# Kernel optimization log

Measured on AMD Instinct MI355X. Metric: run time of the kernel, lower is better.

## Reference

```python
import jax, jax.numpy as jnp
import numpy as np

B, N, D_IN, D_OUT = 16, 2048, 256, 256

def setup_inputs() -> dict:
    key = jax.random.key(0)
    k1, k2, k3 = jax.random.split(key, 3)
    nodes_rep = jax.random.normal(k1, (B, N, D_IN), dtype=jnp.float32)
    adj_metric = jax.random.uniform(k2, (B, N, N), dtype=jnp.float32)
    # xavier_uniform for [D_IN, D_OUT]
    limit = float(np.sqrt(6.0 / (D_IN + D_OUT)))
    attn_weight = jax.random.uniform(k3, (D_IN, D_OUT), dtype=jnp.float32, minval=-limit, maxval=limit)
    attn_bias = jnp.zeros((D_OUT,), dtype=jnp.float32)
    return {"nodes_rep": nodes_rep, "adj_metric": adj_metric,
            "attn_weight": attn_weight, "attn_bias": attn_bias}

def reference(nodes_rep, adj_metric, attn_weight, attn_bias):
    # h: [B, N, D_OUT]
    h = jnp.einsum('bni,io->bno', nodes_rep, attn_weight)
    # scores: [B, N, N]
    scores = jnp.einsum('bno,bmo->bnm', h, h)
    scores = jax.nn.leaky_relu(scores, negative_slope=0.2)
    scores = scores * adj_metric
    attn = jax.nn.softmax(scores, axis=-1)
    # output aggregates the UNtransformed input, then adds bias
    out = jnp.einsum('bnm,bmd->bnd', attn, nodes_rep) + attn_bias
    return out
```

## Files before the change

### kernel.cpp

```cpp
#include <hip/hip_runtime.h>
#include <math.h>
#include <stdint.h>

typedef _Float16 half8 __attribute__((ext_vector_type(8)));
typedef _Float16 half2v __attribute__((ext_vector_type(2)));
typedef float    f32x4 __attribute__((ext_vector_type(4)));
typedef unsigned int uint4v __attribute__((ext_vector_type(4)));

constexpr int Bc = 16, Nn = 2048, Dd = 256;
constexpr int QTI = 64;
constexpr int MC  = 64;

__device__ _Float16 g_Wt[Dd * Dd];

__global__ void __launch_bounds__(256)
wt_transpose_kernel(const float* __restrict__ W) {
    __shared__ float ts[64][65];
    const int t = threadIdx.x;
    const int r0 = blockIdx.x * 64;
    const int c0 = blockIdx.y * 64;
    for (int idx = t; idx < 64 * 64; idx += 256) {
        const int i = idx >> 6, j = idx & 63;
        ts[i][j] = W[(r0 + i) * Dd + c0 + j];
    }
    __syncthreads();
    for (int idx = t; idx < 64 * 64; idx += 256) {
        const int c = idx >> 6, rl = idx & 63;
        g_Wt[(c0 + c) * Dd + r0 + rl] = (_Float16)ts[rl][c];
    }
}

__global__ void __launch_bounds__(256)
nodes_transpose_kernel(const float* __restrict__ nodes, _Float16* __restrict__ vt) {
    __shared__ float ts[64][65];
    const int t  = threadIdx.x;
    const int n0 = blockIdx.x * 64;
    const int d0 = blockIdx.y * 64;
    const int b  = blockIdx.z;
    const float* src = nodes + (size_t)b * Nn * Dd;
    _Float16*    dst = vt    + (size_t)b * Dd * Nn;
    for (int idx = t; idx < 64 * 64; idx += 256) {
        const int i = idx >> 6, j = idx & 63;
        ts[i][j] = src[(size_t)(n0 + i) * Dd + d0 + j];
    }
    __syncthreads();
    for (int idx = t; idx < 64 * 64; idx += 256) {
        const int d = idx >> 6, nl = idx & 63;
        dst[(size_t)(d0 + d) * Nn + n0 + nl] = (_Float16)ts[nl][d];
    }
}

__global__ void __launch_bounds__(256, 2)
hgemm_kernel(const float* __restrict__ nodes, _Float16* __restrict__ h16) {
    __shared__ _Float16 Wt_s[128][264];
    const int t = threadIdx.x, w = t >> 6, lane = t & 63;
    const int quad = lane >> 4, l16 = lane & 15;
    const size_t row0 = (size_t)blockIdx.x * 64 + 16 * w;

    half8 aq[8];
    {
        const float* src = nodes + (row0 + l16) * Dd + quad * 8;
        #pragma unroll
        for (int kf = 0; kf < 8; ++kf) {
            const f32x4 a0 = *(const f32x4*)(src + kf * 32);
            const f32x4 a1 = *(const f32x4*)(src + kf * 32 + 4);
            half8 a;
            a[0] = (_Float16)a0[0]; a[1] = (_Float16)a0[1];
            a[2] = (_Float16)a0[2]; a[3] = (_Float16)a0[3];
            a[4] = (_Float16)a1[0]; a[5] = (_Float16)a1[1];
            a[6] = (_Float16)a1[2]; a[7] = (_Float16)a1[3];
            aq[kf] = a;
        }
    }
    f32x4 acc[16];
    #pragma unroll
    for (int ot = 0; ot < 16; ++ot) acc[ot] = (f32x4){0.f, 0.f, 0.f, 0.f};

    #pragma unroll
    for (int hh = 0; hh < 2; ++hh) {
        if (hh) __syncthreads();
        #pragma unroll
        for (int ii = 0; ii < 16; ++ii) {
            const int i = t + ii * 256;
            *(half8*)&Wt_s[i >> 5][(i & 31) * 8] =
                *(const half8*)&g_Wt[(size_t)(hh * 128 + (i >> 5)) * Dd + (i & 31) * 8];
        }
        __syncthreads();
        #pragma unroll
        for (int kf = 0; kf < 8; ++kf)
            #pragma unroll
            for (int ot = 0; ot < 8; ++ot) {
                const half8 bw = *(const half8*)&Wt_s[ot * 16 + l16][kf * 32 + quad * 8];
                acc[hh * 8 + ot] = __builtin_amdgcn_mfma_f32_16x16x32_f16(aq[kf], bw, acc[hh * 8 + ot], 0, 0, 0);
            }
    }
    #pragma unroll
    for (int idx = 0; idx < 16; ++idx) {
        const int hh = idx >> 3, ot = idx & 7;
        #pragma unroll
        for (int r = 0; r < 4; ++r)
            h16[(row0 + quad * 4 + r) * Dd + hh * 128 + ot * 16 + l16] = (_Float16)acc[idx][r];
    }
}

__global__ void __launch_bounds__(256, 2)
gat_attn_kernel(const _Float16* __restrict__ h, const _Float16* __restrict__ vt,
                const float* __restrict__ adj, const float* __restrict__ bias,
                float* __restrict__ out) {
    __shared__ __align__(16) char lds_raw[70656];
    _Float16 (*hm_s)[264] = (_Float16 (*)[264])lds_raw;
    _Float16 (*V_s)[72]   = (_Float16 (*)[72])(lds_raw + 33792);
    float (*tw)[16][69]   = (float (*)[16][69])lds_raw;

    const int t = threadIdx.x, w = t >> 6, lane = t & 63;
    const int quad = lane >> 4, l16 = lane & 15;
    const int b  = blockIdx.x & 15;
    const int q0 = (blockIdx.x >> 4) * QTI;

    const _Float16* hb = h   + (size_t)b * Nn * Dd;
    const _Float16* vb = vt  + (size_t)b * Dd * Nn;
    const float*   abq = adj + ((size_t)b * Nn + (q0 + 16 * w + l16)) * Nn;

    half8 hmr[8], vr[8];
    #pragma unroll
    for (int ii = 0; ii < 8; ++ii) {
        const int i = t + ii * 256;
        hmr[ii] = *(const half8*)(hb + (size_t)(i >> 5) * Dd + (i & 31) * 8);
        vr[ii]  = *(const half8*)(vb + (size_t)(i >> 3) * Nn + (i & 7) * 8);
    }
    f32x4 adjr[4];
    #pragma unroll
    for (int mt = 0; mt < 4; ++mt)
        adjr[mt] = *(const f32x4*)(abq + mt * 16 + quad * 4);

    half8 bq[8];
    {
        const _Float16* s = hb + (size_t)(q0 + 16 * w + l16) * Dd + quad * 8;
        #pragma unroll
        for (int kf = 0; kf < 8; ++kf) bq[kf] = *(const half8*)(s + kf * 32);
    }

    f32x4 ot_[16];
    #pragma unroll
    for (int dt = 0; dt < 16; ++dt) ot_[dt] = (f32x4){0.f, 0.f, 0.f, 0.f};
    float m_run = -1e30f, l_run = 0.f;

    const int s0 = ((lane >> 4) & 1) * 32 + l16;
    const int s1 = s0 + 16;
    const bool qlow = lane < 32;

    #pragma unroll
    for (int ii = 0; ii < 8; ++ii) {
        const int i = t + ii * 256;
        *(half8*)&hm_s[i >> 5][(i & 31) * 8] = hmr[ii];
        *(half8*)&V_s[i >> 3][(i & 7) * 8]   = vr[ii];
    }
    #pragma unroll
    for (int ii = 0; ii < 8; ++ii) {
        const int i = t + ii * 256;
        hmr[ii] = *(const half8*)(hb + (size_t)(MC + (i >> 5)) * Dd + (i & 31) * 8);
        vr[ii]  = *(const half8*)(vb + (size_t)(i >> 3) * Nn + MC + (i & 7) * 8);
    }
    asm volatile("s_waitcnt lgkmcnt(0)" ::: "memory");
    __builtin_amdgcn_s_barrier();
    asm volatile("" ::: "memory");

    for (int mb = 0; mb < Nn; mb += MC) {
        f32x4 st[4];
        #pragma unroll
        for (int mt = 0; mt < 4; ++mt) st[mt] = (f32x4){0.f, 0.f, 0.f, 0.f};
        __builtin_amdgcn_s_setprio(1);
        #pragma unroll
        for (int kf = 0; kf < 8; ++kf)
            #pragma unroll
            for (int mt = 0; mt < 4; ++mt) {
                const half8 am = *(const half8*)&hm_s[mt * 16 + l16][kf * 32 + quad * 8];
                st[mt] = __builtin_amdgcn_mfma_f32_16x16x32_f16(am, bq[kf], st[mt], 0, 0, 0);
            }
        __builtin_amdgcn_s_setprio(0);

        float rm = -1e30f;
        #pragma unroll
        for (int mt = 0; mt < 4; ++mt) {
            const f32x4 a4 = adjr[mt];
            #pragma unroll
            for (int r = 0; r < 4; ++r) {
                float s = st[mt][r];
                s = (s >= 0.f) ? s : 0.2f * s;
                s *= a4[r];
                st[mt][r] = s;
                rm = fmaxf(rm, s);
            }
        }
        if (mb + MC < Nn) {
            #pragma unroll
            for (int mt = 0; mt < 4; ++mt)
                adjr[mt] = *(const f32x4*)(abq + mb + MC + mt * 16 + quad * 4);
        }
        rm = fmaxf(rm, __shfl_xor(rm, 16));
        rm = fmaxf(rm, __shfl_xor(rm, 32));
        const float mn    = fmaxf(m_run, rm);
        const float alpha = __expf(m_run - mn);
        m_run = mn;
        float rs = 0.f;
        #pragma unroll
        for (int mt = 0; mt < 4; ++mt)
            #pragma unroll
            for (int r = 0; r < 4; ++r) {
                const float p = __expf(st[mt][r] - mn);
                st[mt][r] = p;
                rs += p;
            }
        rs += __shfl_xor(rs, 16);
        rs += __shfl_xor(rs, 32);
        l_run = l_run * alpha + rs;

        #pragma unroll
        for (int dt = 0; dt < 16; ++dt) {
            ot_[dt][0] *= alpha; ot_[dt][1] *= alpha;
            ot_[dt][2] *= alpha; ot_[dt][3] *= alpha;
        }

        uint32_t pk[4][2];
        #pragma unroll
        for (int mt = 0; mt < 4; ++mt) {
            half2v h01, h23;
            h01[0] = (_Float16)st[mt][0]; h01[1] = (_Float16)st[mt][1];
            h23[0] = (_Float16)st[mt][2]; h23[1] = (_Float16)st[mt][3];
            pk[mt][0] = __builtin_bit_cast(uint32_t, h01);
            pk[mt][1] = __builtin_bit_cast(uint32_t, h23);
        }

        #pragma unroll
        for (int ks = 0; ks < 2; ++ks) {
            uint4v bw_;
            {
                const int mA = 2 * ks, mB = 2 * ks + 1;
                const uint32_t a00 = (uint32_t)__shfl((int)pk[mA][0], s0);
                const uint32_t b00 = (uint32_t)__shfl((int)pk[mB][0], s0);
                const uint32_t a10 = (uint32_t)__shfl((int)pk[mA][1], s0);
                const uint32_t b10 = (uint32_t)__shfl((int)pk[mB][1], s0);
                const uint32_t a01 = (uint32_t)__shfl((int)pk[mA][0], s1);
                const uint32_t b01 = (uint32_t)__shfl((int)pk[mB][0], s1);
                const uint32_t a11 = (uint32_t)__shfl((int)pk[mA][1], s1);
                const uint32_t b11 = (uint32_t)__shfl((int)pk[mB][1], s1);
                bw_[0] = qlow ? a00 : b00;
                bw_[1] = qlow ? a10 : b10;
                bw_[2] = qlow ? a01 : b01;
                bw_[3] = qlow ? a11 : b11;
            }
            const half8 bp = __builtin_bit_cast(half8, bw_);
            __builtin_amdgcn_s_setprio(1);
            #pragma unroll
            for (int dt = 0; dt < 16; ++dt) {
                const half8 va = *(const half8*)&V_s[dt * 16 + l16][ks * 32 + quad * 8];
                ot_[dt] = __builtin_amdgcn_mfma_f32_16x16x32_f16(va, bp, ot_[dt], 0, 0, 0);
            }
            __builtin_amdgcn_s_setprio(0);
        }

        if (mb + MC < Nn) {
            asm volatile("" ::: "memory");
            __builtin_amdgcn_s_barrier();
            asm volatile("" ::: "memory");
            #pragma unroll
            for (int ii = 0; ii < 8; ++ii) {
                const int i = t + ii * 256;
                *(half8*)&hm_s[i >> 5][(i & 31) * 8] = hmr[ii];
                *(half8*)&V_s[i >> 3][(i & 7) * 8]   = vr[ii];
            }
            if (mb + 2 * MC < Nn) {
                #pragma unroll
                for (int ii = 0; ii < 8; ++ii) {
                    const int i = t + ii * 256;
                    hmr[ii] = *(const half8*)(hb + (size_t)(mb + 2 * MC + (i >> 5)) * Dd + (i & 31) * 8);
                    vr[ii]  = *(const half8*)(vb + (size_t)(i >> 3) * Nn + mb + 2 * MC + (i & 7) * 8);
                }
            }
            asm volatile("s_waitcnt lgkmcnt(0)" ::: "memory");
            __builtin_amdgcn_s_barrier();
            asm volatile("" ::: "memory");
        }
    }

    __syncthreads();
    const float invl = 1.f / l_run;
    #pragma unroll
    for (int dt = 0; dt < 16; ++dt) {
        ot_[dt][0] *= invl; ot_[dt][1] *= invl;
        ot_[dt][2] *= invl; ot_[dt][3] *= invl;
    }
    float* T = &tw[w][0][0];
    const int rr = lane >> 2, cg = lane & 3;
    float* orow = out + ((size_t)b * Nn + q0 + 16 * w + rr) * Dd;
    #pragma unroll
    for (int dc = 0; dc < 4; ++dc) {
        #pragma unroll
        for (int k4 = 0; k4 < 4; ++k4) {
            const int dt = dc * 4 + k4;
            #pragma unroll
            for (int r = 0; r < 4; ++r)
                T[l16 * 69 + k4 * 16 + quad * 4 + r] = ot_[dt][r];
        }
        asm volatile("s_waitcnt lgkmcnt(0)" ::: "memory");
        #pragma unroll
        for (int c = 0; c < 4; ++c) {
            f32x4 v;
            #pragma unroll
            for (int e = 0; e < 4; ++e) v[e] = T[rr * 69 + cg * 16 + 4 * c + e];
            const int d = dc * 64 + cg * 16 + 4 * c;
            const f32x4 bs = *(const f32x4*)(bias + d);
            v[0] += bs[0]; v[1] += bs[1]; v[2] += bs[2]; v[3] += bs[3];
            *(f32x4*)(orow + d) = v;
        }
        asm volatile("s_waitcnt lgkmcnt(0)" ::: "memory");
    }
}

extern "C" void kernel_launch(void* const* d_in, const int* in_sizes, int n_in,
                              void* d_out, int out_size, void* d_ws, size_t ws_size,
                              hipStream_t stream) {
    const float* nodes = (const float*)d_in[0];
    const float* adj   = (const float*)d_in[1];
    const float* W     = (const float*)d_in[2];
    const float* bias  = (const float*)d_in[3];
    float* out = (float*)d_out;

    _Float16* h16 = (_Float16*)d_ws;
    _Float16* vtp = h16 + (size_t)Bc * Nn * Dd;

    hipLaunchKernelGGL(wt_transpose_kernel, dim3(4, 4), dim3(256), 0, stream, W);
    hipLaunchKernelGGL(nodes_transpose_kernel, dim3(32, 4, 16), dim3(256), 0, stream, nodes, vtp);
    hipLaunchKernelGGL(hgemm_kernel, dim3(512), dim3(256), 0, stream, nodes, h16);
    hipLaunchKernelGGL(gat_attn_kernel, dim3(512), dim3(256), 0, stream, h16, vtp, adj, bias, out);
}
```

Measured before the change: 566.7 us.

## Double query tile per block with async LDS loads, swizzle, and lazy rescale

Each wave now handles two 16-row query tiles, so every K/V fragment read from LDS feeds two MFMAs, and the grid is halved to 256 blocks with one block per CU. K and V chunks are double-buffered in LDS through global_load_lds with an XOR swizzle, replacing the register staging and padded layout. The online-softmax rescale of the accumulators is skipped when no row max grows. The costs are much higher register and LDS use, lower occupancy, and only 256 blocks to spread across the CUs.

```diff
diff --git a/kernel.cpp b/kernel.cpp
--- a/kernel.cpp
+++ b/kernel.cpp
@@ -8,10 +8,16 @@
 typedef unsigned int uint4v __attribute__((ext_vector_type(4)));
 
 constexpr int Bc = 16, Nn = 2048, Dd = 256;
-constexpr int QTI = 64;
+constexpr int QTI = 128;
 constexpr int MC  = 64;
 
 __device__ _Float16 g_Wt[Dd * Dd];
+
+__device__ __forceinline__ void gload16(const void* g, void* l) {
+    __builtin_amdgcn_global_load_lds(
+        (const __attribute__((address_space(1))) void*)g,
+        (__attribute__((address_space(3))) void*)l, 16, 0, 0);
+}
 
 __global__ void __launch_bounds__(256)
 wt_transpose_kernel(const float* __restrict__ W) {
@@ -103,14 +109,16 @@
     }
 }
 
-__global__ void __launch_bounds__(256, 2)
+__global__ void __launch_bounds__(256, 1)
 gat_attn_kernel(const _Float16* __restrict__ h, const _Float16* __restrict__ vt,
                 const float* __restrict__ adj, const float* __restrict__ bias,
                 float* __restrict__ out) {
-    __shared__ __align__(16) char lds_raw[70656];
-    _Float16 (*hm_s)[264] = (_Float16 (*)[264])lds_raw;
-    _Float16 (*V_s)[72]   = (_Float16 (*)[72])(lds_raw + 33792);
-    float (*tw)[16][69]   = (float (*)[16][69])lds_raw;
+    __shared__ __align__(16) char lds_raw[131072];
+    _Float16* hmA = (_Float16*)lds_raw;
+    _Float16* hmBuf = (_Float16*)(lds_raw + 32768);
+    _Float16* vA  = (_Float16*)(lds_raw + 65536);
+    _Float16* vBuf = (_Float16*)(lds_raw + 98304);
+    auto tw = (float (*)[16][69])lds_raw;
 
     const int t = threadIdx.x, w = t >> 6, lane = t & 63;
     const int quad = lane >> 4, l16 = lane & 15;
@@ -119,202 +127,217 @@
 
     const _Float16* hb = h   + (size_t)b * Nn * Dd;
     const _Float16* vb = vt  + (size_t)b * Dd * Nn;
-    const float*   abq = adj + ((size_t)b * Nn + (q0 + 16 * w + l16)) * Nn;
-
-    half8 hmr[8], vr[8];
+    const float* abq0 = adj + ((size_t)b * Nn + (q0 + 32 * w + l16)) * Nn;
+    const float* abq1 = abq0 + (size_t)16 * Nn;
+
     #pragma unroll
     for (int ii = 0; ii < 8; ++ii) {
         const int i = t + ii * 256;
-        hmr[ii] = *(const half8*)(hb + (size_t)(i >> 5) * Dd + (i & 31) * 8);
-        vr[ii]  = *(const half8*)(vb + (size_t)(i >> 3) * Nn + (i & 7) * 8);
-    }
-    f32x4 adjr[4];
-    #pragma unroll
-    for (int mt = 0; mt < 4; ++mt)
-        adjr[mt] = *(const f32x4*)(abq + mt * 16 + quad * 4);
-
-    half8 bq[8];
+        const int mp = i >> 5, s = i & 31;
+        gload16(hb + (size_t)mp * Dd + ((s ^ (mp & 7)) * 8), hmA + i * 8);
+    }
+    #pragma unroll
+    for (int ii = 0; ii < 8; ++ii) {
+        const int i = t + ii * 256;
+        const int dp = i >> 3, s = i & 7;
+        gload16(vb + (size_t)dp * Nn + ((s ^ (dp & 7)) * 8), vA + i * 8);
+    }
+    f32x4 adjA0[4], adjA1[4], adjB0[4], adjB1[4];
+    #pragma unroll
+    for (int mt = 0; mt < 4; ++mt) {
+        adjA0[mt] = *(const f32x4*)(abq0 + mt * 16 + quad * 4);
+        adjA1[mt] = *(const f32x4*)(abq1 + mt * 16 + quad * 4);
+    }
+
+    half8 bq0[8], bq1[8];
     {
-        const _Float16* s = hb + (size_t)(q0 + 16 * w + l16) * Dd + quad * 8;
-        #pragma unroll
-        for (int kf = 0; kf < 8; ++kf) bq[kf] = *(const half8*)(s + kf * 32);
-    }
-
-    f32x4 ot_[16];
-    #pragma unroll
-    for (int dt = 0; dt < 16; ++dt) ot_[dt] = (f32x4){0.f, 0.f, 0.f, 0.f};
-    float m_run = -1e30f, l_run = 0.f;
+        const _Float16* s0p = hb + (size_t)(q0 + 32 * w + l16) * Dd + quad * 8;
+        #pragma unroll
+        for (int kf = 0; kf < 8; ++kf) {
+            bq0[kf] = *(const half8*)(s0p + kf * 32);
+            bq1[kf] = *(const half8*)(s0p + 16 * Dd + kf * 32);
+        }
+    }
+
+    f32x4 o0[16], o1[16];
+    #pragma unroll
+    for (int dt = 0; dt < 16; ++dt) {
+        o0[dt] = (f32x4){0.f, 0.f, 0.f, 0.f};
+        o1[dt] = (f32x4){0.f, 0.f, 0.f, 0.f};
+    }
+    float m0 = -1e30f, l0 = 0.f, m1 = -1e30f, l1 = 0.f;
 
     const int s0 = ((lane >> 4) & 1) * 32 + l16;
     const int s1 = s0 + 16;
     const bool qlow = lane < 32;
 
-    #pragma unroll
-    for (int ii = 0; ii < 8; ++ii) {
-        const int i = t + ii * 256;
-        *(half8*)&hm_s[i >> 5][(i & 31) * 8] = hmr[ii];
-        *(half8*)&V_s[i >> 3][(i & 7) * 8]   = vr[ii];
-    }
-    #pragma unroll
-    for (int ii = 0; ii < 8; ++ii) {
-        const int i = t + ii * 256;
-        hmr[ii] = *(const half8*)(hb + (size_t)(MC + (i >> 5)) * Dd + (i & 31) * 8);
-        vr[ii]  = *(const half8*)(vb + (size_t)(i >> 3) * Nn + MC + (i & 7) * 8);
-    }
-    asm volatile("s_waitcnt lgkmcnt(0)" ::: "memory");
-    __builtin_amdgcn_s_barrier();
-    asm volatile("" ::: "memory");
-
-    for (int mb = 0; mb < Nn; mb += MC) {
-        f32x4 st[4];
-        #pragma unroll
-        for (int mt = 0; mt < 4; ++mt) st[mt] = (f32x4){0.f, 0.f, 0.f, 0.f};
-        __builtin_amdgcn_s_setprio(1);
-        #pragma unroll
-        for (int kf = 0; kf < 8; ++kf)
-            #pragma unroll
-            for (int mt = 0; mt < 4; ++mt) {
-                const half8 am = *(const half8*)&hm_s[mt * 16 + l16][kf * 32 + quad * 8];
-                st[mt] = __builtin_amdgcn_mfma_f32_16x16x32_f16(am, bq[kf], st[mt], 0, 0, 0);
-            }
-        __builtin_amdgcn_s_setprio(0);
-
+    __syncthreads();
+
+    auto sm = [&](f32x4 (&stq)[4], const f32x4 (&aj)[4], float& mr, float& lr,
+                  uint32_t (&pk)[4][2], f32x4 (&o)[16]) {
         float rm = -1e30f;
         #pragma unroll
-        for (int mt = 0; mt < 4; ++mt) {
-            const f32x4 a4 = adjr[mt];
+        for (int mt = 0; mt < 4; ++mt)
             #pragma unroll
             for (int r = 0; r < 4; ++r) {
-                float s = st[mt][r];
+                float s = stq[mt][r];
                 s = (s >= 0.f) ? s : 0.2f * s;
-                s *= a4[r];
-                st[mt][r] = s;
+                s *= aj[mt][r];
+                stq[mt][r] = s;
                 rm = fmaxf(rm, s);
             }
-        }
-        if (mb + MC < Nn) {
-            #pragma unroll
-            for (int mt = 0; mt < 4; ++mt)
-                adjr[mt] = *(const f32x4*)(abq + mb + MC + mt * 16 + quad * 4);
-        }
         rm = fmaxf(rm, __shfl_xor(rm, 16));
         rm = fmaxf(rm, __shfl_xor(rm, 32));
-        const float mn    = fmaxf(m_run, rm);
-        const float alpha = __expf(m_run - mn);
-        m_run = mn;
+        if (!__all(rm <= mr)) {
+            const float mn    = fmaxf(mr, rm);
+            const float alpha = __expf(mr - mn);
+            mr = mn;
+            lr *= alpha;
+            #pragma unroll
+            for (int dt = 0; dt < 16; ++dt) {
+                o[dt][0] *= alpha; o[dt][1] *= alpha;
+                o[dt][2] *= alpha; o[dt][3] *= alpha;
+            }
+        }
         float rs = 0.f;
         #pragma unroll
         for (int mt = 0; mt < 4; ++mt)
             #pragma unroll
             for (int r = 0; r < 4; ++r) {
-                const float p = __expf(st[mt][r] - mn);
-                st[mt][r] = p;
+                const float p = __expf(stq[mt][r] - mr);
+                stq[mt][r] = p;
                 rs += p;
             }
         rs += __shfl_xor(rs, 16);
         rs += __shfl_xor(rs, 32);
-        l_run = l_run * alpha + rs;
-
-        #pragma unroll
-        for (int dt = 0; dt < 16; ++dt) {
-            ot_[dt][0] *= alpha; ot_[dt][1] *= alpha;
-            ot_[dt][2] *= alpha; ot_[dt][3] *= alpha;
-        }
-
-        uint32_t pk[4][2];
+        lr += rs;
         #pragma unroll
         for (int mt = 0; mt < 4; ++mt) {
             half2v h01, h23;
-            h01[0] = (_Float16)st[mt][0]; h01[1] = (_Float16)st[mt][1];
-            h23[0] = (_Float16)st[mt][2]; h23[1] = (_Float16)st[mt][3];
+            h01[0] = (_Float16)stq[mt][0]; h01[1] = (_Float16)stq[mt][1];
+            h23[0] = (_Float16)stq[mt][2]; h23[1] = (_Float16)stq[mt][3];
             pk[mt][0] = __builtin_bit_cast(uint32_t, h01);
             pk[mt][1] = __builtin_bit_cast(uint32_t, h23);
         }
-
-        #pragma unroll
-        for (int ks = 0; ks < 2; ++ks) {
-            uint4v bw_;
-            {
-                const int mA = 2 * ks, mB = 2 * ks + 1;
-                const uint32_t a00 = (uint32_t)__shfl((int)pk[mA][0], s0);
-                const uint32_t b00 = (uint32_t)__shfl((int)pk[mB][0], s0);
-                const uint32_t a10 = (uint32_t)__shfl((int)pk[mA][1], s0);
-                const uint32_t b10 = (uint32_t)__shfl((int)pk[mB][1], s0);
-                const uint32_t a01 = (uint32_t)__shfl((int)pk[mA][0], s1);
-                const uint32_t b01 = (uint32_t)__shfl((int)pk[mB][0], s1);
-                const uint32_t a11 = (uint32_t)__shfl((int)pk[mA][1], s1);
-                const uint32_t b11 = (uint32_t)__shfl((int)pk[mB][1], s1);
-                bw_[0] = qlow ? a00 : b00;
-                bw_[1] = qlow ? a10 : b10;
-                bw_[2] = qlow ? a01 : b01;
-                bw_[3] = qlow ? a11 : b11;
-            }
-            const half8 bp = __builtin_bit_cast(half8, bw_);
-            __builtin_amdgcn_s_setprio(1);
-            #pragma unroll
-            for (int dt = 0; dt < 16; ++dt) {
-                const half8 va = *(const half8*)&V_s[dt * 16 + l16][ks * 32 + quad * 8];
-                ot_[dt] = __builtin_amdgcn_mfma_f32_16x16x32_f16(va, bp, ot_[dt], 0, 0, 0);
-            }
-            __builtin_amdgcn_s_setprio(0);
-        }
-
-        if (mb + MC < Nn) {
-            asm volatile("" ::: "memory");
-            __builtin_amdgcn_s_barrier();
-            asm volatile("" ::: "memory");
+    };
+    auto redist = [&](const uint32_t (&pk)[4][2], int ks) -> half8 {
+        const int mA = 2 * ks, mB = 2 * ks + 1;
+        uint4v bw_;
+        const uint32_t a00 = (uint32_t)__shfl((int)pk[mA][0], s0);
+        const uint32_t b00 = (uint32_t)__shfl((int)pk[mB][0], s0);
+        const uint32_t a10 = (uint32_t)__shfl((int)pk[mA][1], s0);
+        const uint32_t b10 = (uint32_t)__shfl((int)pk[mB][1], s0);
+        const uint32_t a01 = (uint32_t)__shfl((int)pk[mA][0], s1);
+        const uint32_t b01 = (uint32_t)__shfl((int)pk[mB][0], s1);
+        const uint32_t a11 = (uint32_t)__shfl((int)pk[mA][1], s1);
+        const uint32_t b11 = (uint32_t)__shfl((int)pk[mB][1], s1);
+        bw_[0] = qlow ? a00 : b00;
+        bw_[1] = qlow ? a10 : b10;
+        bw_[2] = qlow ? a01 : b01;
+        bw_[3] = qlow ? a11 : b11;
+        return __builtin_bit_cast(half8, bw_);
+    };
+
+    auto chunk = [&](const _Float16* hmC, const _Float16* vC,
+                     _Float16* hmN, _Float16* vN,
+                     const f32x4 (&ac0)[4], const f32x4 (&ac1)[4],
+                     f32x4 (&an0)[4], f32x4 (&an1)[4], int mb) {
+        const int mb2 = mb + MC;
+        if (mb2 < Nn) {
             #pragma unroll
             for (int ii = 0; ii < 8; ++ii) {
                 const int i = t + ii * 256;
-                *(half8*)&hm_s[i >> 5][(i & 31) * 8] = hmr[ii];
-                *(half8*)&V_s[i >> 3][(i & 7) * 8]   = vr[ii];
-            }
-            if (mb + 2 * MC < Nn) {
+                const int mp = i >> 5, s = i & 31;
+                gload16(hb + (size_t)(mb2 + mp) * Dd + ((s ^ (mp & 7)) * 8), hmN + i * 8);
+            }
+            #pragma unroll
+            for (int ii = 0; ii < 8; ++ii) {
+                const int i = t + ii * 256;
+                const int dp = i >> 3, s = i & 7;
+                gload16(vb + (size_t)dp * Nn + mb2 + ((s ^ (dp & 7)) * 8), vN + i * 8);
+            }
+            #pragma unroll
+            for (int mt = 0; mt < 4; ++mt) {
+                an0[mt] = *(const f32x4*)(abq0 + mb2 + mt * 16 + quad * 4);
+                an1[mt] = *(const f32x4*)(abq1 + mb2 + mt * 16 + quad * 4);
+            }
+        }
+
+        f32x4 st0[4], st1[4];
+        #pragma unroll
+        for (int mt = 0; mt < 4; ++mt) {
+            st0[mt] = (f32x4){0.f, 0.f, 0.f, 0.f};
+            st1[mt] = (f32x4){0.f, 0.f, 0.f, 0.f};
+        }
+        #pragma unroll
+        for (int kf = 0; kf < 8; ++kf)
+            #pragma unroll
+            for (int mt = 0; mt < 4; ++mt) {
+                const int m  = mt * 16 + l16;
+                const int pg = (kf * 4 + quad) ^ (m & 7);
+                const half8 am = *(const half8*)(hmC + m * 256 + pg * 8);
+                st0[mt] = __builtin_amdgcn_mfma_f32_16x16x32_f16(am, bq0[kf], st0[mt], 0, 0, 0);
+                st1[mt] = __builtin_amdgcn_mfma_f32_16x16x32_f16(am, bq1[kf], st1[mt], 0, 0, 0);
+            }
+
+        uint32_t pk0[4][2], pk1[4][2];
+        sm(st0, ac0, m0, l0, pk0, o0);
+        sm(st1, ac1, m1, l1, pk1, o1);
+
+        #pragma unroll
+        for (int ks = 0; ks < 2; ++ks) {
+            const half8 bp0 = redist(pk0, ks);
+            const half8 bp1 = redist(pk1, ks);
+            #pragma unroll
+            for (int dt = 0; dt < 16; ++dt) {
+                const int d  = dt * 16 + l16;
+                const int pg = (ks * 4 + quad) ^ (d & 7);
+                const half8 va = *(const half8*)(vC + d * 64 + pg * 8);
+                o0[dt] = __builtin_amdgcn_mfma_f32_16x16x32_f16(va, bp0, o0[dt], 0, 0, 0);
+                o1[dt] = __builtin_amdgcn_mfma_f32_16x16x32_f16(va, bp1, o1[dt], 0, 0, 0);
+            }
+        }
+        __syncthreads();
+    };
+
+    for (int mb = 0; mb < Nn; mb += 2 * MC) {
+        chunk(hmA, vA, hmBuf, vBuf, adjA0, adjA1, adjB0, adjB1, mb);
+        chunk(hmBuf, vBuf, hmA, vA, adjB0, adjB1, adjA0, adjA1, mb + MC);
+    }
+
+    auto epi = [&](f32x4 (&o)[16], float lr, int qrow) {
+        const float invl = 1.f / lr;
+        #pragma unroll
+        for (int dt = 0; dt < 16; ++dt) {
+            o[dt][0] *= invl; o[dt][1] *= invl;
+            o[dt][2] *= invl; o[dt][3] *= invl;
+        }
+        float* T = &tw[w][0][0];
+        const int rr = lane >> 2, cg = lane & 3;
+        float* orow = out + ((size_t)b * Nn + qrow + rr) * Dd;
+        #pragma unroll
+        for (int dc = 0; dc < 4; ++dc) {
+            #pragma unroll
+            for (int k4 = 0; k4 < 4; ++k4)
                 #pragma unroll
-                for (int ii = 0; ii < 8; ++ii) {
-                    const int i = t + ii * 256;
-                    hmr[ii] = *(const half8*)(hb + (size_t)(mb + 2 * MC + (i >> 5)) * Dd + (i & 31) * 8);
-                    vr[ii]  = *(const half8*)(vb + (size_t)(i >> 3) * Nn + mb + 2 * MC + (i & 7) * 8);
-                }
-            }
+                for (int r = 0; r < 4; ++r)
+                    T[l16 * 69 + k4 * 16 + quad * 4 + r] = o[dc * 4 + k4][r];
             asm volatile("s_waitcnt lgkmcnt(0)" ::: "memory");
-            __builtin_amdgcn_s_barrier();
-            asm volatile("" ::: "memory");
-        }
-    }
-
-    __syncthreads();
-    const float invl = 1.f / l_run;
-    #pragma unroll
-    for (int dt = 0; dt < 16; ++dt) {
-        ot_[dt][0] *= invl; ot_[dt][1] *= invl;
-        ot_[dt][2] *= invl; ot_[dt][3] *= invl;
-    }
-    float* T = &tw[w][0][0];
-    const int rr = lane >> 2, cg = lane & 3;
-    float* orow = out + ((size_t)b * Nn + q0 + 16 * w + rr) * Dd;
-    #pragma unroll
-    for (int dc = 0; dc < 4; ++dc) {
-        #pragma unroll
-        for (int k4 = 0; k4 < 4; ++k4) {
-            const int dt = dc * 4 + k4;
-            #pragma unroll
-            for (int r = 0; r < 4; ++r)
-                T[l16 * 69 + k4 * 16 + quad * 4 + r] = ot_[dt][r];
-        }
-        asm volatile("s_waitcnt lgkmcnt(0)" ::: "memory");
-        #pragma unroll
-        for (int c = 0; c < 4; ++c) {
-            f32x4 v;
-            #pragma unroll
-            for (int e = 0; e < 4; ++e) v[e] = T[rr * 69 + cg * 16 + 4 * c + e];
-            const int d = dc * 64 + cg * 16 + 4 * c;
-            const f32x4 bs = *(const f32x4*)(bias + d);
-            v[0] += bs[0]; v[1] += bs[1]; v[2] += bs[2]; v[3] += bs[3];
-            *(f32x4*)(orow + d) = v;
-        }
-        asm volatile("s_waitcnt lgkmcnt(0)" ::: "memory");
-    }
+            #pragma unroll
+            for (int c = 0; c < 4; ++c) {
+                f32x4 v;
+                #pragma unroll
+                for (int e = 0; e < 4; ++e) v[e] = T[rr * 69 + cg * 16 + 4 * c + e];
+                const int d = dc * 64 + cg * 16 + 4 * c;
+                const f32x4 bs = *(const f32x4*)(bias + d);
+                v[0] += bs[0]; v[1] += bs[1]; v[2] += bs[2]; v[3] += bs[3];
+                *(f32x4*)(orow + d) = v;
+            }
+            asm volatile("s_waitcnt lgkmcnt(0)" ::: "memory");
+        }
+    };
+    epi(o0, l0, q0 + 32 * w);
+    epi(o1, l1, q0 + 32 * w + 16);
 }
 
 extern "C" void kernel_launch(void* const* d_in, const int* in_sizes, int n_in,
@@ -332,5 +355,5 @@
     hipLaunchKernelGGL(wt_transpose_kernel, dim3(4, 4), dim3(256), 0, stream, W);
     hipLaunchKernelGGL(nodes_transpose_kernel, dim3(32, 4, 16), dim3(256), 0, stream, nodes, vtp);
     hipLaunchKernelGGL(hgemm_kernel, dim3(512), dim3(256), 0, stream, nodes, h16);
-    hipLaunchKernelGGL(gat_attn_kernel, dim3(512), dim3(256), 0, stream, h16, vtp, adj, bias, out);
-}
+    hipLaunchKernelGGL(gat_attn_kernel, dim3(256), dim3(256), 0, stream, h16, vtp, adj, bias, out);
+}
```

Result: slower. 755.6 us (+33.3%).
